# Optimization experiments

Measured on AMD Instinct MI355X. Metric: run time of the kernel, lower is better.

The kernel has to match this reference:

```python
import jax, jax.numpy as jnp
import numpy as np

H = 300          # node_hidden_dim (GINE output dim)
D = 2 * H        # set2set in_channels = 600
STEPS = 2        # num_step_set2_set


def _lstm_cell(x, h, c, W_ih, W_hh, b_ih, b_hh):
    # PyTorch LSTM gate order: i, f, g, o
    gates = x @ W_ih.T + h @ W_hh.T + b_ih + b_hh
    i, f, g, o = jnp.split(gates, 4, axis=-1)
    c = jax.nn.sigmoid(f) * c + jax.nn.sigmoid(i) * jnp.tanh(g)
    h = jax.nn.sigmoid(o) * jnp.tanh(c)
    return h, c


def _set2set(x, batch, num_graphs, W_ih, W_hh, b_ih, b_hh):
    # torch_geometric Set2Set with processing_steps=STEPS, 1-layer LSTM
    B = num_graphs
    q_star = jnp.zeros((B, 2 * D), x.dtype)
    h = jnp.zeros((B, D), x.dtype)
    c = jnp.zeros((B, D), x.dtype)
    for _ in range(STEPS):
        h, c = _lstm_cell(q_star, h, c, W_ih, W_hh, b_ih, b_hh)
        q = h                                   # [B, D]
        e = jnp.sum(x * q[batch], axis=-1)      # [N]
        emax = jax.ops.segment_max(e, batch, num_segments=B)
        a = jnp.exp(e - emax[batch])
        asum = jax.ops.segment_sum(a, batch, num_segments=B)
        a = a / (asum[batch] + 1e-16)           # segment softmax
        r = jax.ops.segment_sum(a[:, None] * x, batch, num_segments=B)
        q_star = jnp.concatenate([q, r], axis=-1)   # [B, 2D]
    return q_star


def _l2norm(x):
    return x / jnp.maximum(jnp.linalg.norm(x, axis=1, keepdims=True), 1e-12)


def setup_inputs() -> dict:
    key = jax.random.key(0)
    ks = jax.random.split(key, 8)
    Nu, Nv, B = 8192, 8192, 256
    solute_x = jax.random.normal(ks[0], (Nu, H), jnp.float32)
    solvent_x = jax.random.normal(ks[1], (Nv, H), jnp.float32)
    solute_batch = jnp.sort(jax.random.randint(ks[2], (Nu,), 0, B)).astype(jnp.int32)
    solvent_batch = jnp.sort(jax.random.randint(ks[3], (Nv,), 0, B)).astype(jnp.int32)
    lstm_W_ih = jax.random.normal(ks[4], (4 * D, 2 * D), jnp.float32) * 0.02
    lstm_W_hh = jax.random.normal(ks[5], (4 * D, D), jnp.float32) * 0.02
    lstm_b_ih = jnp.zeros((4 * D,), jnp.float32)
    lstm_b_hh = jnp.zeros((4 * D,), jnp.float32)
    pred_W = jax.random.normal(ks[6], (1, 8 * H), jnp.float32) * 0.02
    pred_b = jnp.zeros((1,), jnp.float32)
    return {
        "solute_x": solute_x, "solvent_x": solvent_x,
        "solute_batch": solute_batch, "solvent_batch": solvent_batch,
        "num_graphs": B,
        "lstm_W_ih": lstm_W_ih, "lstm_W_hh": lstm_W_hh,
        "lstm_b_ih": lstm_b_ih, "lstm_b_hh": lstm_b_hh,
        "pred_W": pred_W, "pred_b": pred_b,
    }


def reference(solute_x, solvent_x, solute_batch, solvent_batch, num_graphs,
              lstm_W_ih, lstm_W_hh, lstm_b_ih, lstm_b_hh, pred_W, pred_b):
    # F.normalize(dim=1)
    su = _l2norm(solute_x)    # [Nu, H]
    sv = _l2norm(solvent_x)   # [Nv, H]
    # len_map = solute_len.T @ solvent_len == same-pair membership mask
    mask = (solute_batch[:, None] == solvent_batch[None, :]).astype(su.dtype)
    interaction_map = (su @ sv.T) * mask          # [Nu, Nv]
    ret_interaction_map = interaction_map
    solvent_prime = interaction_map.T @ su        # [Nv, H]
    solute_prime = interaction_map @ sv           # [Nu, H]
    su2 = jnp.concatenate([su, solute_prime], axis=1)    # [Nu, 2H]
    sv2 = jnp.concatenate([sv, solvent_prime], axis=1)   # [Nv, 2H]
    su_s2s = _set2set(su2, solute_batch, num_graphs, lstm_W_ih, lstm_W_hh, lstm_b_ih, lstm_b_hh)
    sv_s2s = _set2set(sv2, solvent_batch, num_graphs, lstm_W_ih, lstm_W_hh, lstm_b_ih, lstm_b_hh)
    final = jnp.concatenate([su_s2s, sv_s2s], axis=1)    # [B, 8H]
    predictions = final @ pred_W.T + pred_b              # [B, 1]
    return predictions, ret_interaction_map
```

## Files before the change

kernel.cpp:

```cpp
#include <hip/hip_runtime.h>
#include <math.h>

#define HDIM 300
#define DDIM 600
#define NGR  256

typedef float vf4 __attribute__((ext_vector_type(4)));
typedef float vf2 __attribute__((ext_vector_type(2)));

__device__ __forceinline__ float wred_sum(float v){
  #pragma unroll
  for(int o=32;o;o>>=1) v += __shfl_xor(v,o,64);
  return v;
}
__device__ __forceinline__ float wred_max(float v){
  #pragma unroll
  for(int o=32;o;o>>=1) v = fmaxf(v,__shfl_xor(v,o,64));
  return v;
}
__device__ __forceinline__ float sigm(float x){ return 1.f/(1.f+expf(-x)); }

__device__ __forceinline__ void fill_row(int i, const int* __restrict__ ub,
    const int* __restrict__ voff, float* __restrict__ mapbase, int Nv, int tid){
  int g = ub[i];
  int js = voff[g], je = voff[g+1];
  float* mrow = mapbase + (size_t)i*Nv;
  const vf4 z4 = {0.f,0.f,0.f,0.f};
  int nf4 = Nv >> 2;
  for (int q4=tid; q4<nf4; q4+=256){
    int j0 = q4*4;
    if (j0+4 <= js || j0 >= je){
      __builtin_nontemporal_store(z4, (vf4*)(mrow + j0));
    } else {
      #pragma unroll
      for(int u=0;u<4;u++){ int j=j0+u; if (j<js || j>=je) mrow[j]=0.f; }
    }
  }
}

__global__ __launch_bounds__(256) void k_norm_off(const float* __restrict__ xu,
    const float* __restrict__ xv, float* __restrict__ su, float* __restrict__ sv,
    int Nu, int Nv, const int* __restrict__ ub, const int* __restrict__ vb,
    int* __restrict__ uoff, int* __restrict__ voff,
    const float* __restrict__ b_ih, const float* __restrict__ b_hh,
    float* __restrict__ h1, float* __restrict__ c1,
    const float* __restrict__ pb, float* __restrict__ outp,
    const float* __restrict__ Wih, const float* __restrict__ Whh,
    float* __restrict__ gbase){
  int NBn = (Nu + Nv) >> 2;
  int b = blockIdx.x;
  int tid = threadIdx.x, lane = tid & 63, w = tid >> 6;
  if (b == NBn){
    int t = tid;
    if (t < NGR){
      int lo=0, hi=Nu;
      while(lo<hi){ int m=(lo+hi)>>1; if (ub[m] < t) lo=m+1; else hi=m; }
      uoff[t]=lo;
      lo=0; hi=Nv;
      while(lo<hi){ int m=(lo+hi)>>1; if (vb[m] < t) lo=m+1; else hi=m; }
      voff[t]=lo;
      if (t==0){ uoff[NGR]=Nu; voff[NGR]=Nv; }
      outp[t] = pb[0];
    }
    for (int d=tid; d<DDIM; d+=256){
      float gi = b_ih[d]      + b_hh[d];
      float gg = b_ih[1200+d] + b_hh[1200+d];
      float go = b_ih[1800+d] + b_hh[1800+d];
      float c  = sigm(gi)*tanhf(gg);
      c1[d]=c; h1[d]=sigm(go)*tanhf(c);
    }
    return;
  }
  if (b > NBn){
    __shared__ float h1l[DDIM];
    for (int d=tid; d<DDIM; d+=256){
      float gi = b_ih[d]      + b_hh[d];
      float gg = b_ih[1200+d] + b_hh[1200+d];
      float go = b_ih[1800+d] + b_hh[1800+d];
      float c  = sigm(gi)*tanhf(gg);
      h1l[d]   = sigm(go)*tanhf(c);
    }
    __syncthreads();
    int n = (b - NBn - 1)*4 + w;
    const float* wi = Wih + (size_t)n*1200;
    const float* wh = Whh + (size_t)n*600;
    float s = 0.f;
    for (int k=lane; k<DDIM; k+=64) s += h1l[k]*(wi[k] + wh[k]);
    s = wred_sum(s);
    if (lane==0) gbase[n] = s + b_ih[n] + b_hh[n];
    return;
  }
  int wid = b*4 + w;
  const float* src; float* dst;
  if (wid < Nu){ src = xu + (size_t)wid*HDIM; dst = su + (size_t)wid*HDIM; }
  else         { src = xv + (size_t)(wid-Nu)*HDIM; dst = sv + (size_t)(wid-Nu)*HDIM; }
  const vf4* s4 = (const vf4*)src;
  vf4 A = s4[lane];
  vf4 Bv = (lane<11)? s4[64+lane] : (vf4){0.f,0.f,0.f,0.f};
  float s = A.x*A.x+A.y*A.y+A.z*A.z+A.w*A.w + Bv.x*Bv.x+Bv.y*Bv.y+Bv.z*Bv.z+Bv.w*Bv.w;
  s = wred_sum(s);
  float inv = 1.f / fmaxf(sqrtf(s), 1e-12f);
  vf4* d4 = (vf4*)dst;
  d4[lane] = A*inv;
  if (lane<11) d4[64+lane] = Bv*inv;
}

__global__ __launch_bounds__(256) void k_prime(const float* __restrict__ su,
    const float* __restrict__ sv, const int* __restrict__ ub,
    const int* __restrict__ vb, const int* __restrict__ uoff,
    const int* __restrict__ voff, float* __restrict__ spr,
    float* __restrict__ svp, float* __restrict__ e1u, float* __restrict__ e1v,
    const float* __restrict__ h1, float* __restrict__ mapbase, int Nu, int Nv){
  int b = blockIdx.x;
  int tid = threadIdx.x, lane = tid & 63, w = tid >> 6;
  int r = b % 3;
  if (r == 2){ fill_row(b/3, ub, voff, mapbase, Nv, tid); return; }
  int idx = (b/3)*2 + r;
  bool isU = (idx < Nu);
  int i = isU ? idx : idx - Nu;
  const float* xa = isU ? su : sv;
  const float* xb = isU ? sv : su;
  const int* mybatch = isU ? ub : vb;
  const int* ooff    = isU ? voff : uoff;
  float* prime = isU ? spr : svp;
  float* eout  = isU ? e1u : e1v;

  __shared__ __align__(16) float xrow[304];
  __shared__ __align__(16) float prl[4*304];
  __shared__ float qv[2*HDIM];
  __shared__ float red[4];
  const float* rowp = xa + (size_t)i*HDIM;
  for (int t=tid; t<HDIM;   t+=256) xrow[t] = rowp[t];
  for (int t=tid; t<2*HDIM; t+=256) qv[t]   = h1[t];
  int g = mybatch[i];
  int js = ooff[g], je = ooff[g+1];
  __syncthreads();

  const vf4* x4 = (const vf4*)xrow;
  vf4 xA = x4[lane];
  vf4 xB = (lane<11)? x4[64+lane] : (vf4){0.f,0.f,0.f,0.f};
  vf4 prA = {0.f,0.f,0.f,0.f}, prB = {0.f,0.f,0.f,0.f};
  for (int j = js + w; j < je; j += 4){
    const vf4* orow = (const vf4*)(xb + (size_t)j*HDIM);
    vf4 oA = orow[lane];
    vf4 oB = (lane<11)? orow[64+lane] : (vf4){0.f,0.f,0.f,0.f};
    float d = oA.x*xA.x + oA.y*xA.y + oA.z*xA.z + oA.w*xA.w
            + oB.x*xB.x + oB.y*xB.y + oB.z*xB.z + oB.w*xB.w;
    d = wred_sum(d);
    if (isU && lane==0) mapbase[(size_t)i*Nv + j] = d;
    prA += d * oA;
    prB += d * oB;
  }
  vf4* p4 = (vf4*)(prl + w*304);
  p4[lane] = prA;
  if (lane<11) p4[64+lane] = prB;
  __syncthreads();
  float ep = 0.f;
  for (int t=tid; t<HDIM; t+=256){
    float s = prl[t] + prl[304+t] + prl[608+t] + prl[912+t];
    prime[(size_t)i*HDIM + t] = s;
    ep += xrow[t]*qv[t] + s*qv[HDIM+t];
  }
  ep = wred_sum(ep);
  if (lane==0) red[w] = ep;
  __syncthreads();
  if (tid==0) eout[i] = red[0]+red[1]+red[2]+red[3];
}

__global__ __launch_bounds__(256) void k_r1(const float* __restrict__ su,
    const float* __restrict__ sv, const float* __restrict__ spr,
    const float* __restrict__ svp, const float* __restrict__ e1u,
    const float* __restrict__ e1v, const int* __restrict__ uoff,
    const int* __restrict__ voff, float* __restrict__ r1){
  int tid = threadIdx.x, lane = tid & 63, w = tid >> 6;
  int bs = blockIdx.x; int set = bs >> 8; int g = bs & 255;
  const float* x  = set? sv  : su;
  const float* pr = set? svp : spr;
  const float* e  = set? e1v : e1u;
  const int* off  = set? voff: uoff;
  __shared__ float al[2048]; __shared__ float red[4]; __shared__ float shv;
  int ns = off[g], ne = off[g+1]; int n = ne - ns;
  float m = -INFINITY;
  for (int t=ns+tid; t<ne; t+=256) m = fmaxf(m, e[t]);
  m = wred_max(m);
  if (lane==0) red[w]=m;
  __syncthreads();
  if (tid==0) shv = fmaxf(fmaxf(red[0],red[1]),fmaxf(red[2],red[3]));
  __syncthreads();
  float emax = shv;
  float s = 0.f;
  for (int t=tid; t<n; t+=256){ float a = expf(e[ns+t]-emax); if (t<2048) al[t]=a; s += a; }
  s = wred_sum(s);
  __syncthreads();
  if (lane==0) red[w]=s;
  __syncthreads();
  if (tid==0) shv = red[0]+red[1]+red[2]+red[3];
  __syncthreads();
  float inv = 1.f/(shv + 1e-16f);
  float acc[3] = {0.f,0.f,0.f};
  #pragma unroll 4
  for (int nn=0; nn<n; nn++){
    float a = (nn<2048)? al[nn] : expf(e[ns+nn]-emax);
    const float* xr = x  + (size_t)(ns+nn)*HDIM;
    const float* pp = pr + (size_t)(ns+nn)*HDIM;
    #pragma unroll
    for(int u=0;u<3;u++){ int c = tid + u*256; if (c<DDIM){
        float xv = (c<HDIM)? xr[c] : pp[c-HDIM]; acc[u] += a*xv; } }
  }
  #pragma unroll
  for(int u=0;u<3;u++){ int c = tid + u*256; if (c<DDIM) r1[(size_t)bs*DDIM + c] = acc[u]*inv; }
}

__global__ __launch_bounds__(256) void k_gemm_lstm(const float* __restrict__ r1,
    const float* __restrict__ Wih, const float* __restrict__ gbase,
    const float* __restrict__ c1, float* __restrict__ h2){
  __shared__ __align__(16) float smem[32*68];
  float* Al = smem;
  float* Bl = smem + 16*36;
  int tid = threadIdx.x;
  int d0  = blockIdx.x*16;
  int gs0 = blockIdx.y*32;
  int tx = tid & 15, ty = tid >> 4;
  float acc[2][4] = {};
  for (int kt=0; kt<600; kt+=16){
    int k = kt + tx;
    bool kok = (k < 600);
    #pragma unroll
    for (int u=0; u<2; u++){
      int rl = ty + u*16;
      Al[tx*36 + rl] = kok ? r1[(size_t)(gs0+rl)*DDIM + k] : 0.f;
    }
    #pragma unroll
    for (int u=0; u<4; u++){
      int cl = ty + u*16;
      int gate = cl >> 4, dd = cl & 15;
      int d = d0 + dd;
      Bl[tx*68 + cl] = (kok && d < 600)
          ? Wih[(size_t)(gate*600 + d)*1200 + 600 + k] : 0.f;
    }
    __syncthreads();
    #pragma unroll
    for (int kk=0; kk<16; kk++){
      vf2 av = ((const vf2*)(Al + kk*36))[ty];
      vf4 bv = ((const vf4*)(Bl + kk*68))[tx];
      float a[2]={av.x,av.y}, bb[4]={bv.x,bv.y,bv.z,bv.w};
      #pragma unroll
      for(int mm=0;mm<2;mm++)
        #pragma unroll
        for(int nn=0;nn<4;nn++) acc[mm][nn] += a[mm]*bb[nn];
    }
    __syncthreads();
  }
  #pragma unroll
  for (int mm=0; mm<2; mm++){
    vf4 o = {acc[mm][0], acc[mm][1], acc[mm][2], acc[mm][3]};
    ((vf4*)(smem + (ty*2+mm)*68))[tx] = o;
  }
  __syncthreads();
  int d_l = tid & 15, r0 = tid >> 4;
  int d = d0 + d_l;
  if (d < 600){
    float gb_i = gbase[d], gb_f = gbase[600+d], gb_g = gbase[1200+d], gb_o = gbase[1800+d];
    float cc1 = c1[d];
    #pragma unroll
    for (int u=0; u<2; u++){
      int rl = r0 + u*16;
      const float* gr = smem + rl*68;
      float gi = gr[d_l]      + gb_i;
      float gf = gr[16+d_l]   + gb_f;
      float gG = gr[32+d_l]   + gb_g;
      float go = gr[48+d_l]   + gb_o;
      float c  = sigm(gf)*cc1 + sigm(gi)*tanhf(gG);
      h2[(size_t)(gs0+rl)*DDIM + d] = sigm(go)*tanhf(c);
    }
  }
}

__global__ __launch_bounds__(256) void k_r2(const float* __restrict__ su,
    const float* __restrict__ sv, const float* __restrict__ spr,
    const float* __restrict__ svp, const int* __restrict__ uoff,
    const int* __restrict__ voff, const float* __restrict__ h2,
    const float* __restrict__ pW, float* __restrict__ e2u,
    float* __restrict__ e2v, float* __restrict__ outp){
  int tid = threadIdx.x, lane = tid & 63, w = tid >> 6;
  int bs = blockIdx.x; int set = bs >> 8; int g = bs & 255;
  const float* x  = set? sv  : su;
  const float* pr = set? svp : spr;
  const int* off  = set? voff: uoff;
  float* e2g      = set? e2v : e2u;
  __shared__ float q[DDIM]; __shared__ float e2l[128]; __shared__ float al[128];
  __shared__ float red[4]; __shared__ float shv;
  for (int t=tid; t<DDIM; t+=256) q[t] = h2[(size_t)bs*DDIM + t];
  int ns = off[g], ne = off[g+1]; int n = ne - ns;
  __syncthreads();
  #pragma unroll 2
  for (int node = ns + w; node < ne; node += 4){
    const float* xr = x  + (size_t)node*HDIM;
    const float* pp = pr + (size_t)node*HDIM;
    float d = 0.f;
    #pragma unroll
    for(int c=0;c<10;c++){ int k = lane + 64*c; if (k<DDIM){
        float xv = (k<HDIM)? xr[k] : pp[k-HDIM]; d += xv*q[k]; } }
    d = wred_sum(d);
    if (lane==0){ int t = node-ns; if (t<128) e2l[t] = d; else e2g[node] = d; }
  }
  __syncthreads();
  float m = -INFINITY;
  for (int t=tid; t<n; t+=256) m = fmaxf(m, (t<128)? e2l[t] : e2g[ns+t]);
  m = wred_max(m);
  if (lane==0) red[w]=m;
  __syncthreads();
  if (tid==0) shv = fmaxf(fmaxf(red[0],red[1]),fmaxf(red[2],red[3]));
  __syncthreads();
  float emax = shv;
  float s = 0.f;
  for (int t=tid; t<n; t+=256){
    float a = expf(((t<128)? e2l[t] : e2g[ns+t]) - emax);
    if (t<128) al[t]=a; else e2g[ns+t]=a;
    s += a;
  }
  s = wred_sum(s);
  __syncthreads();
  if (lane==0) red[w]=s;
  __syncthreads();
  if (tid==0) shv = red[0]+red[1]+red[2]+red[3];
  __syncthreads();
  float inv = 1.f/(shv + 1e-16f);
  float acc[3] = {0.f,0.f,0.f};
  #pragma unroll 4
  for (int nn=0; nn<n; nn++){
    float a = (nn<128)? al[nn] : e2g[ns+nn];
    const float* xr = x  + (size_t)(ns+nn)*HDIM;
    const float* pp = pr + (size_t)(ns+nn)*HDIM;
    #pragma unroll
    for(int u=0;u<3;u++){ int c = tid + u*256; if (c<DDIM){
        float xv = (c<HDIM)? xr[c] : pp[c-HDIM]; acc[u] += a*xv; } }
  }
  int hoff = set? 1200 : 0;
  float p = 0.f;
  #pragma unroll
  for(int u=0;u<3;u++){ int c = tid + u*256; if (c<DDIM) p += (acc[u]*inv)*pW[hoff+600+c]; }
  for (int t=tid; t<DDIM; t+=256) p += q[t]*pW[hoff+t];
  p = wred_sum(p);
  __syncthreads();
  if (lane==0) red[w] = p;
  __syncthreads();
  if (tid==0) atomicAdd(&outp[g], red[0]+red[1]+red[2]+red[3]);
}

extern "C" void kernel_launch(void* const* d_in, const int* in_sizes, int n_in,
                              void* d_out, int out_size, void* d_ws, size_t ws_size,
                              hipStream_t stream) {
  const float* solute_x  = (const float*)d_in[0];
  const float* solvent_x = (const float*)d_in[1];
  const int*   ub        = (const int*)d_in[2];
  const int*   vb        = (const int*)d_in[3];
  const float* Wih  = (const float*)d_in[5];
  const float* Whh  = (const float*)d_in[6];
  const float* b_ih = (const float*)d_in[7];
  const float* b_hh = (const float*)d_in[8];
  const float* pW   = (const float*)d_in[9];
  const float* pb   = (const float*)d_in[10];

  int Nu = in_sizes[0] / HDIM;
  int Nv = in_sizes[1] / HDIM;

  float* out = (float*)d_out;
  int predn = out_size - Nu*Nv;
  float* mapbase = out + predn;

  float* ws = (float*)d_ws;
  float* su    = ws;
  float* sv    = su    + (size_t)Nu*HDIM;
  float* spr   = sv    + (size_t)Nv*HDIM;
  float* svp   = spr   + (size_t)Nu*HDIM;
  float* e1u   = svp   + (size_t)Nv*HDIM;
  float* e1v   = e1u   + Nu;
  float* h1    = e1v   + Nv;
  float* c1    = h1    + DDIM;
  float* r1    = c1    + DDIM;
  float* gbase = r1    + 512*DDIM;
  float* h2    = gbase + 2400;
  int*   uoff  = (int*)(h2 + 512*DDIM);
  int*   voff  = uoff + 257;

  k_norm_off<<<dim3((Nu+Nv)/4 + 1 + 600), dim3(256), 0, stream>>>(
      solute_x, solvent_x, su, sv, Nu, Nv, ub, vb, uoff, voff,
      b_ih, b_hh, h1, c1, pb, out, Wih, Whh, gbase);
  k_prime<<<dim3(24576), dim3(256), 0, stream>>>(
      su, sv, ub, vb, uoff, voff, spr, svp, e1u, e1v, h1, mapbase, Nu, Nv);
  k_r1<<<dim3(512), dim3(256), 0, stream>>>(
      su, sv, spr, svp, e1u, e1v, uoff, voff, r1);
  k_gemm_lstm<<<dim3(38, 16), dim3(256), 0, stream>>>(r1, Wih, gbase, c1, h2);
  k_r2<<<dim3(512), dim3(256), 0, stream>>>(
      su, sv, spr, svp, uoff, voff, h2, pW, e1u, e1v, out);
}
```

Baseline: 520.9 us.

## Fuse per-row prime computation and first set2set readout into per-graph blocks

Replaces the per-row k_prime kernel and the per-graph k_r1 kernel with one k_graph kernel. Each of 512 compute blocks handles one graph of one set. It stages the partner graph's rows in shared memory in tiles of 32 and processes the block's own rows eight at a time, so partner rows are reused across many rows instead of being reloaded for each row. The same block then does the segment softmax and the first weighted readout, which removes a kernel launch and the global round trip of e1. Map-row filling blocks are interleaved into the same grid. The cost is only 512 large blocks plus long serial loops per graph, which can hurt occupancy and load balance, and the interleaving index arithmetic is intricate.

Measured after the change: 583.2 us. +12.0%, slower.

```diff
diff --git a/kernel.cpp b/kernel.cpp
--- a/kernel.cpp
+++ b/kernel.cpp
@@ -105,83 +105,152 @@
   if (lane<11) d4[64+lane] = Bv*inv;
 }
 
-__global__ __launch_bounds__(256) void k_prime(const float* __restrict__ su,
-    const float* __restrict__ sv, const int* __restrict__ ub,
-    const int* __restrict__ vb, const int* __restrict__ uoff,
-    const int* __restrict__ voff, float* __restrict__ spr,
-    float* __restrict__ svp, float* __restrict__ e1u, float* __restrict__ e1v,
-    const float* __restrict__ h1, float* __restrict__ mapbase, int Nu, int Nv){
+__global__ __launch_bounds__(256) void k_graph(
+    const float* __restrict__ su, const float* __restrict__ sv,
+    const int* __restrict__ ub,
+    const int* __restrict__ uoff, const int* __restrict__ voff,
+    float* __restrict__ spr, float* __restrict__ svp,
+    float* __restrict__ e1u, float* __restrict__ e1v,
+    const float* __restrict__ h1, float* __restrict__ mapbase,
+    float* __restrict__ r1, int Nv){
   int b = blockIdx.x;
   int tid = threadIdx.x, lane = tid & 63, w = tid >> 6;
-  int r = b % 3;
-  if (r == 2){ fill_row(b/3, ub, voff, mapbase, Nv, tid); return; }
-  int idx = (b/3)*2 + r;
-  bool isU = (idx < Nu);
-  int i = isU ? idx : idx - Nu;
-  const float* xa = isU ? su : sv;
-  const float* xb = isU ? sv : su;
-  const int* mybatch = isU ? ub : vb;
-  const int* ooff    = isU ? voff : uoff;
-  float* prime = isU ? spr : svp;
-  float* eout  = isU ? e1u : e1v;
-
-  __shared__ __align__(16) float xrow[304];
-  __shared__ __align__(16) float prl[4*304];
-  __shared__ float qv[2*HDIM];
+  int P = (gridDim.x + 511) >> 9;
+  int q = b / P;
+  if ((b % P) != 0 || q >= 512){
+    int nb_comp = (b % P) ? (q + 1) : q;
+    if (nb_comp > 512) nb_comp = 512;
+    fill_row(b - nb_comp, ub, voff, mapbase, Nv, tid);
+    return;
+  }
+  int cid = q;
+  int set = cid & 1, g = cid >> 1;
+  const float* xown = set ? sv  : su;
+  const float* xpar = set ? su  : sv;
+  const int*   ooff = set ? voff: uoff;
+  const int*   poff = set ? uoff: voff;
+  float* prime = set ? svp : spr;
+  float* e1g   = set ? e1v : e1u;
+  int us = ooff[g], ue = ooff[g+1];
+  int ps = poff[g], pe = poff[g+1];
+  int n = ue - us, np = pe - ps;
+
+  __shared__ __align__(16) float SVl[32*308];
+  __shared__ __align__(16) float XUl[8*308];
+  __shared__ __align__(16) float Ql[608];
+  __shared__ float e1l[256];
+  __shared__ float al[256];
   __shared__ float red[4];
-  const float* rowp = xa + (size_t)i*HDIM;
-  for (int t=tid; t<HDIM;   t+=256) xrow[t] = rowp[t];
-  for (int t=tid; t<2*HDIM; t+=256) qv[t]   = h1[t];
-  int g = mybatch[i];
-  int js = ooff[g], je = ooff[g+1];
-  __syncthreads();
-
-  const vf4* x4 = (const vf4*)xrow;
-  vf4 xA = x4[lane];
-  vf4 xB = (lane<11)? x4[64+lane] : (vf4){0.f,0.f,0.f,0.f};
-  vf4 prA = {0.f,0.f,0.f,0.f}, prB = {0.f,0.f,0.f,0.f};
-  for (int j = js + w; j < je; j += 4){
-    const vf4* orow = (const vf4*)(xb + (size_t)j*HDIM);
-    vf4 oA = orow[lane];
-    vf4 oB = (lane<11)? orow[64+lane] : (vf4){0.f,0.f,0.f,0.f};
-    float d = oA.x*xA.x + oA.y*xA.y + oA.z*xA.z + oA.w*xA.w
-            + oB.x*xB.x + oB.y*xB.y + oB.z*xB.z + oB.w*xB.w;
-    d = wred_sum(d);
-    if (isU && lane==0) mapbase[(size_t)i*Nv + j] = d;
-    prA += d * oA;
-    prB += d * oB;
-  }
-  vf4* p4 = (vf4*)(prl + w*304);
-  p4[lane] = prA;
-  if (lane<11) p4[64+lane] = prB;
-  __syncthreads();
-  float ep = 0.f;
-  for (int t=tid; t<HDIM; t+=256){
-    float s = prl[t] + prl[304+t] + prl[608+t] + prl[912+t];
-    prime[(size_t)i*HDIM + t] = s;
-    ep += xrow[t]*qv[t] + s*qv[HDIM+t];
-  }
-  ep = wred_sum(ep);
-  if (lane==0) red[w] = ep;
-  __syncthreads();
-  if (tid==0) eout[i] = red[0]+red[1]+red[2]+red[3];
-}
-
-__global__ __launch_bounds__(256) void k_r1(const float* __restrict__ su,
-    const float* __restrict__ sv, const float* __restrict__ spr,
-    const float* __restrict__ svp, const float* __restrict__ e1u,
-    const float* __restrict__ e1v, const int* __restrict__ uoff,
-    const int* __restrict__ voff, float* __restrict__ r1){
-  int tid = threadIdx.x, lane = tid & 63, w = tid >> 6;
-  int bs = blockIdx.x; int set = bs >> 8; int g = bs & 255;
-  const float* x  = set? sv  : su;
-  const float* pr = set? svp : spr;
-  const float* e  = set? e1v : e1u;
-  const int* off  = set? voff: uoff;
-  __shared__ float al[2048]; __shared__ float red[4]; __shared__ float shv;
-  int ns = off[g], ne = off[g+1]; int n = ne - ns;
+  __shared__ float shv;
+
+  for (int t=tid; t<DDIM; t+=256) Ql[t] = h1[t];
+  bool single = (np <= 32);
+  if (single){
+    for (int idx=tid; idx<np*HDIM; idx+=256){
+      int r = idx/HDIM, c = idx - r*HDIM;
+      SVl[r*308+c] = xpar[(size_t)(ps+r)*HDIM + c];
+    }
+  }
+  const vf4* SV4 = (const vf4*)SVl;
+  const vf4* XU4 = (const vf4*)XUl;
+  const vf4* Q4  = (const vf4*)Ql;
+  int jj = lane & 31, half = lane >> 5;
+
+  int passes = (n + 7) >> 3;
+  for (int p=0; p<passes; p++){
+    int i0 = us + p*8;
+    int nr = min(8, ue - i0);
+    __syncthreads();
+    for (int idx=tid; idx<nr*HDIM; idx+=256){
+      int r = idx/HDIM, c = idx - r*HDIM;
+      XUl[r*308+c] = xown[(size_t)(i0+r)*HDIM + c];
+    }
+    if (!single){
+      int nc0 = np < 32 ? np : 32;
+      for (int idx=tid; idx<nc0*HDIM; idx+=256){
+        int r = idx/HDIM, c = idx - r*HDIM;
+        SVl[r*308+c] = xpar[(size_t)(ps+r)*HDIM + c];
+      }
+    }
+    __syncthreads();
+
+    int lr = 2*w + half;
+    int gi = i0 + lr;
+    bool rv = (lr < nr);
+    vf4 prA0={0,0,0,0}, prB0={0,0,0,0}, prA1={0,0,0,0}, prB1={0,0,0,0};
+
+    for (int cs = ps, ci = 0; cs < pe; cs += 32, ci++){
+      int nc = min(32, pe - cs);
+      if (!single && ci > 0){
+        __syncthreads();
+        for (int idx=tid; idx<nc*HDIM; idx+=256){
+          int r = idx/HDIM, c = idx - r*HDIM;
+          SVl[r*308+c] = xpar[(size_t)(cs+r)*HDIM + c];
+        }
+        __syncthreads();
+      }
+      float d = 0.f;
+      const vf4* svr = SV4 + jj*77;
+      const vf4* xr4 = XU4 + lr*77;
+      for (int c4=0; c4<75; c4++){
+        vf4 s4 = svr[c4], x4 = xr4[c4];
+        d += s4.x*x4.x + s4.y*x4.y + s4.z*x4.z + s4.w*x4.w;
+      }
+      if (set==0 && rv && jj<nc) mapbase[(size_t)gi*Nv + (cs+jj)] = d;
+      for (int j=0; j<nc; j++){
+        float d0 = __shfl(d, j);
+        float d1 = __shfl(d, 32+j);
+        vf4 sA = SV4[j*77 + lane];
+        vf4 sB = (lane<11)? SV4[j*77 + 64 + lane] : (vf4){0,0,0,0};
+        prA0 += d0*sA; prB0 += d0*sB;
+        prA1 += d1*sA; prB1 += d1*sB;
+      }
+    }
+
+    int r0 = 2*w;
+    bool rv0 = (r0   < nr);
+    bool rv1 = (r0+1 < nr);
+    if (rv0){
+      int gi0 = i0 + r0;
+      vf4 xA = XU4[r0*77 + lane];
+      vf4 qA = Q4[lane], q2A = Q4[75+lane];
+      float ep = xA.x*qA.x+xA.y*qA.y+xA.z*qA.z+xA.w*qA.w
+               + prA0.x*q2A.x+prA0.y*q2A.y+prA0.z*q2A.z+prA0.w*q2A.w;
+      if (lane<11){
+        vf4 xB = XU4[r0*77+64+lane];
+        vf4 qB = Q4[64+lane], q2B = Q4[139+lane];
+        ep += xB.x*qB.x+xB.y*qB.y+xB.z*qB.z+xB.w*qB.w
+            + prB0.x*q2B.x+prB0.y*q2B.y+prB0.z*q2B.z+prB0.w*q2B.w;
+      }
+      ep = wred_sum(ep);
+      vf4* p4 = (vf4*)(prime + (size_t)gi0*HDIM);
+      p4[lane] = prA0;
+      if (lane<11) p4[64+lane] = prB0;
+      if (lane==0){ int t = gi0-us; if (t<256) e1l[t]=ep; else e1g[gi0]=ep; }
+    }
+    if (rv1){
+      int gi1 = i0 + r0 + 1;
+      vf4 xA = XU4[(r0+1)*77 + lane];
+      vf4 qA = Q4[lane], q2A = Q4[75+lane];
+      float ep = xA.x*qA.x+xA.y*qA.y+xA.z*qA.z+xA.w*qA.w
+               + prA1.x*q2A.x+prA1.y*q2A.y+prA1.z*q2A.z+prA1.w*q2A.w;
+      if (lane<11){
+        vf4 xB = XU4[(r0+1)*77+64+lane];
+        vf4 qB = Q4[64+lane], q2B = Q4[139+lane];
+        ep += xB.x*qB.x+xB.y*qB.y+xB.z*qB.z+xB.w*qB.w
+            + prB1.x*q2B.x+prB1.y*q2B.y+prB1.z*q2B.z+prB1.w*q2B.w;
+      }
+      ep = wred_sum(ep);
+      vf4* p4 = (vf4*)(prime + (size_t)gi1*HDIM);
+      p4[lane] = prA1;
+      if (lane<11) p4[64+lane] = prB1;
+      if (lane==0){ int t = gi1-us; if (t<256) e1l[t]=ep; else e1g[gi1]=ep; }
+    }
+  }
+
+  __syncthreads();
   float m = -INFINITY;
-  for (int t=ns+tid; t<ne; t+=256) m = fmaxf(m, e[t]);
+  for (int t=tid; t<n; t+=256) m = fmaxf(m, (t<256)? e1l[t] : e1g[us+t]);
   m = wred_max(m);
   if (lane==0) red[w]=m;
   __syncthreads();
@@ -189,7 +258,11 @@
   __syncthreads();
   float emax = shv;
   float s = 0.f;
-  for (int t=tid; t<n; t+=256){ float a = expf(e[ns+t]-emax); if (t<2048) al[t]=a; s += a; }
+  for (int t=tid; t<n; t+=256){
+    float a = expf(((t<256)? e1l[t] : e1g[us+t]) - emax);
+    if (t<256) al[t]=a; else e1g[us+t]=a;
+    s += a;
+  }
   s = wred_sum(s);
   __syncthreads();
   if (lane==0) red[w]=s;
@@ -200,13 +273,14 @@
   float acc[3] = {0.f,0.f,0.f};
   #pragma unroll 4
   for (int nn=0; nn<n; nn++){
-    float a = (nn<2048)? al[nn] : expf(e[ns+nn]-emax);
-    const float* xr = x  + (size_t)(ns+nn)*HDIM;
-    const float* pp = pr + (size_t)(ns+nn)*HDIM;
+    float a = (nn<256)? al[nn] : e1g[us+nn];
+    const float* xr = xown  + (size_t)(us+nn)*HDIM;
+    const float* pp = prime + (size_t)(us+nn)*HDIM;
     #pragma unroll
     for(int u=0;u<3;u++){ int c = tid + u*256; if (c<DDIM){
         float xv = (c<HDIM)? xr[c] : pp[c-HDIM]; acc[u] += a*xv; } }
   }
+  int bs = (set<<8) | g;
   #pragma unroll
   for(int u=0;u<3;u++){ int c = tid + u*256; if (c<DDIM) r1[(size_t)bs*DDIM + c] = acc[u]*inv; }
 }
@@ -387,10 +461,8 @@
   k_norm_off<<<dim3((Nu+Nv)/4 + 1 + 600), dim3(256), 0, stream>>>(
       solute_x, solvent_x, su, sv, Nu, Nv, ub, vb, uoff, voff,
       b_ih, b_hh, h1, c1, pb, out, Wih, Whh, gbase);
-  k_prime<<<dim3(24576), dim3(256), 0, stream>>>(
-      su, sv, ub, vb, uoff, voff, spr, svp, e1u, e1v, h1, mapbase, Nu, Nv);
-  k_r1<<<dim3(512), dim3(256), 0, stream>>>(
-      su, sv, spr, svp, e1u, e1v, uoff, voff, r1);
+  k_graph<<<dim3(Nu + 512), dim3(256), 0, stream>>>(
+      su, sv, ub, uoff, voff, spr, svp, e1u, e1v, h1, mapbase, r1, Nv);
   k_gemm_lstm<<<dim3(38, 16), dim3(256), 0, stream>>>(r1, Wih, gbase, c1, h2);
   k_r2<<<dim3(512), dim3(256), 0, stream>>>(
       su, sv, spr, svp, uoff, voff, h2, pW, e1u, e1v, out);
```

## Process two rows per wave with lane-parallel dot products in pair kernel

Applied to the files above, without the earlier changes.

Replaces the per-row prime kernel with a pair kernel in which each wave handles two consecutive rows. The dot products are computed one partner row per lane, then broadcast with shuffles to accumulate the prime vectors, so each partner row load is shared by both rows. Blocks that fill map rows are interleaved with compute blocks. The goal is to cut repeated partner loads and the per-dot wave reductions, at the cost of strided per-lane loads and more divergence when a row pair straddles two graphs.

After: 569.1 us. 9.3% more time.

```diff
diff --git a/kernel.cpp b/kernel.cpp
--- a/kernel.cpp
+++ b/kernel.cpp
@@ -105,66 +105,106 @@
   if (lane<11) d4[64+lane] = Bv*inv;
 }
 
-__global__ __launch_bounds__(256) void k_prime(const float* __restrict__ su,
-    const float* __restrict__ sv, const int* __restrict__ ub,
-    const int* __restrict__ vb, const int* __restrict__ uoff,
-    const int* __restrict__ voff, float* __restrict__ spr,
-    float* __restrict__ svp, float* __restrict__ e1u, float* __restrict__ e1v,
-    const float* __restrict__ h1, float* __restrict__ mapbase, int Nu, int Nv){
-  int b = blockIdx.x;
-  int tid = threadIdx.x, lane = tid & 63, w = tid >> 6;
-  int r = b % 3;
-  if (r == 2){ fill_row(b/3, ub, voff, mapbase, Nv, tid); return; }
-  int idx = (b/3)*2 + r;
-  bool isU = (idx < Nu);
-  int i = isU ? idx : idx - Nu;
-  const float* xa = isU ? su : sv;
-  const float* xb = isU ? sv : su;
-  const int* mybatch = isU ? ub : vb;
-  const int* ooff    = isU ? voff : uoff;
-  float* prime = isU ? spr : svp;
-  float* eout  = isU ? e1u : e1v;
-
-  __shared__ __align__(16) float xrow[304];
-  __shared__ __align__(16) float prl[4*304];
-  __shared__ float qv[2*HDIM];
-  __shared__ float red[4];
-  const float* rowp = xa + (size_t)i*HDIM;
-  for (int t=tid; t<HDIM;   t+=256) xrow[t] = rowp[t];
-  for (int t=tid; t<2*HDIM; t+=256) qv[t]   = h1[t];
-  int g = mybatch[i];
-  int js = ooff[g], je = ooff[g+1];
-  __syncthreads();
-
-  const vf4* x4 = (const vf4*)xrow;
-  vf4 xA = x4[lane];
-  vf4 xB = (lane<11)? x4[64+lane] : (vf4){0.f,0.f,0.f,0.f};
-  vf4 prA = {0.f,0.f,0.f,0.f}, prB = {0.f,0.f,0.f,0.f};
-  for (int j = js + w; j < je; j += 4){
-    const vf4* orow = (const vf4*)(xb + (size_t)j*HDIM);
-    vf4 oA = orow[lane];
-    vf4 oB = (lane<11)? orow[64+lane] : (vf4){0.f,0.f,0.f,0.f};
-    float d = oA.x*xA.x + oA.y*xA.y + oA.z*xA.z + oA.w*xA.w
-            + oB.x*xB.x + oB.y*xB.y + oB.z*xB.z + oB.w*xB.w;
-    d = wred_sum(d);
-    if (isU && lane==0) mapbase[(size_t)i*Nv + j] = d;
-    prA += d * oA;
-    prB += d * oB;
-  }
-  vf4* p4 = (vf4*)(prl + w*304);
-  p4[lane] = prA;
-  if (lane<11) p4[64+lane] = prB;
-  __syncthreads();
-  float ep = 0.f;
-  for (int t=tid; t<HDIM; t+=256){
-    float s = prl[t] + prl[304+t] + prl[608+t] + prl[912+t];
-    prime[(size_t)i*HDIM + t] = s;
-    ep += xrow[t]*qv[t] + s*qv[HDIM+t];
-  }
-  ep = wred_sum(ep);
-  if (lane==0) red[w] = ep;
-  __syncthreads();
-  if (tid==0) eout[i] = red[0]+red[1]+red[2]+red[3];
+__global__ __launch_bounds__(256) void k_pair(
+    const float* __restrict__ su, const float* __restrict__ sv,
+    const int* __restrict__ ub, const int* __restrict__ vb,
+    const int* __restrict__ uoff, const int* __restrict__ voff,
+    float* __restrict__ spr, float* __restrict__ svp,
+    float* __restrict__ e1u, float* __restrict__ e1v,
+    const float* __restrict__ h1, float* __restrict__ mapbase,
+    int Nu, int Nv){
+  int b = blockIdx.x, tid = threadIdx.x, lane = tid & 63, w = tid >> 6;
+  int ncomp = (Nu + Nv) >> 3;
+  int P = gridDim.x / ncomp;
+  int q = b / P;
+  if ((b % P) != 0 || q >= ncomp){
+    int nb = (b % P) ? (q + 1) : q;
+    if (nb > ncomp) nb = ncomp;
+    fill_row(b - nb, ub, voff, mapbase, Nv, tid);
+    return;
+  }
+  int p  = q*4 + w;
+  int r0 = 2*p;
+  bool isU = (r0 < Nu);
+  int i0 = isU ? r0 : r0 - Nu;
+  const float* xown = isU ? su : sv;
+  const float* xpar = isU ? sv : su;
+  const int* batch  = isU ? ub : vb;
+  const int* poff   = isU ? voff : uoff;
+  float* prime      = isU ? spr : svp;
+  float* e1g        = isU ? e1u : e1v;
+
+  __shared__ __align__(16) float XS[4][2*308];
+  float* X = XS[w];
+  for (int t=lane; t<2*HDIM; t+=64){
+    int rr = t / HDIM, c = t - rr*HDIM;
+    X[rr*308 + c] = xown[(size_t)i0*HDIM + t];
+  }
+  int g0 = batch[i0], g1 = batch[i0+1];
+  int ngrp = (g0==g1) ? 1 : 2;
+  const vf4* H4  = (const vf4*)h1;
+  const vf4* H4b = (const vf4*)(h1 + HDIM);
+
+  for (int grp=0; grp<ngrp; grp++){
+    int g  = grp ? g1 : g0;
+    int rA = (ngrp==2) ? grp : 0;
+    int has2 = (ngrp==1) ? 1 : 0;
+    int ps = poff[g], pe = poff[g+1];
+    const vf4* X0 = (const vf4*)(X + rA*308);
+    const vf4* X1 = (const vf4*)(X + (rA+1)*308);
+    vf4 pA0={0,0,0,0}, pB0={0,0,0,0}, pA1={0,0,0,0}, pB1={0,0,0,0};
+    for (int cs=ps; cs<pe; cs+=64){
+      int nc = min(64, pe-cs);
+      float d0 = 0.f, d1 = 0.f;
+      if (lane < nc){
+        const vf4* pr = (const vf4*)(xpar + (size_t)(cs+lane)*HDIM);
+        #pragma unroll 5
+        for (int c4=0; c4<75; c4++){
+          vf4 pv = pr[c4];
+          vf4 x0 = X0[c4];
+          d0 += pv.x*x0.x + pv.y*x0.y + pv.z*x0.z + pv.w*x0.w;
+          if (has2){
+            vf4 x1 = X1[c4];
+            d1 += pv.x*x1.x + pv.y*x1.y + pv.z*x1.z + pv.w*x1.w;
+          }
+        }
+      }
+      if (isU && lane < nc){
+        mapbase[(size_t)(i0+rA)*Nv + (cs+lane)] = d0;
+        if (has2) mapbase[(size_t)(i0+rA+1)*Nv + (cs+lane)] = d1;
+      }
+      for (int j=0; j<nc; j++){
+        float dj0 = __shfl(d0, j);
+        float dj1 = has2 ? __shfl(d1, j) : 0.f;
+        const vf4* pr = (const vf4*)(xpar + (size_t)(cs+j)*HDIM);
+        vf4 a  = pr[lane];
+        vf4 bb = (lane<11) ? pr[64+lane] : (vf4){0.f,0.f,0.f,0.f};
+        pA0 += dj0*a; pB0 += dj0*bb;
+        if (has2){ pA1 += dj1*a; pB1 += dj1*bb; }
+      }
+    }
+    for (int rr=0; rr<=has2; rr++){
+      int irow = i0 + rA + rr;
+      vf4 pA = rr ? pA1 : pA0;
+      vf4 pB = rr ? pB1 : pB0;
+      vf4* pp = (vf4*)(prime + (size_t)irow*HDIM);
+      pp[lane] = pA;
+      if (lane<11) pp[64+lane] = pB;
+      const vf4* Xr = (const vf4*)(X + (rA+rr)*308);
+      vf4 xo = Xr[lane];
+      vf4 q1 = H4[lane], q2 = H4b[lane];
+      float ep = xo.x*q1.x+xo.y*q1.y+xo.z*q1.z+xo.w*q1.w
+               + pA.x*q2.x+pA.y*q2.y+pA.z*q2.z+pA.w*q2.w;
+      if (lane<11){
+        vf4 xo2 = Xr[64+lane];
+        vf4 q1b = H4[64+lane], q2b = H4b[64+lane];
+        ep += xo2.x*q1b.x+xo2.y*q1b.y+xo2.z*q1b.z+xo2.w*q1b.w
+            + pB.x*q2b.x+pB.y*q2b.y+pB.z*q2b.z+pB.w*q2b.w;
+      }
+      ep = wred_sum(ep);
+      if (lane==0) e1g[irow] = ep;
+    }
+  }
 }
 
 __global__ __launch_bounds__(256) void k_r1(const float* __restrict__ su,
@@ -387,7 +427,7 @@
   k_norm_off<<<dim3((Nu+Nv)/4 + 1 + 600), dim3(256), 0, stream>>>(
       solute_x, solvent_x, su, sv, Nu, Nv, ub, vb, uoff, voff,
       b_ih, b_hh, h1, c1, pb, out, Wih, Whh, gbase);
-  k_prime<<<dim3(24576), dim3(256), 0, stream>>>(
+  k_pair<<<dim3((Nu+Nv)/8 + Nu), dim3(256), 0, stream>>>(
       su, sv, ub, vb, uoff, voff, spr, svp, e1u, e1v, h1, mapbase, Nu, Nv);
   k_r1<<<dim3(512), dim3(256), 0, stream>>>(
       su, sv, spr, svp, e1u, e1v, uoff, voff, r1);
```

## Fuse five kernel stages into one cooperative persistent kernel with grid syncs

Applied to the files above, without the earlier changes.

Replaces the five separate launches (normalize/offsets, prime/interaction map, r1, LSTM GEMM, r2) with one cooperative kernel of 1024 blocks. The blocks loop over virtual block indices and separate the stages with grid-wide syncs. The aim is to remove launch overhead and the gaps between kernels. In exchange, occupancy is capped by the cooperative grid size and the large stages run as grid-stride loops, which may balance load worse. The original multi-launch path is kept as a fallback if the cooperative launch fails.

After: 1.048 ms. 101% more time.

```diff
diff --git a/kernel.cpp b/kernel.cpp
--- a/kernel.cpp
+++ b/kernel.cpp
@@ -1,9 +1,12 @@
 #include <hip/hip_runtime.h>
+#include <hip/hip_cooperative_groups.h>
 #include <math.h>
 
 #define HDIM 300
 #define DDIM 600
 #define NGR  256
+
+namespace cg = cooperative_groups;
 
 typedef float vf4 __attribute__((ext_vector_type(4)));
 typedef float vf2 __attribute__((ext_vector_type(2)));
@@ -35,6 +38,315 @@
       #pragma unroll
       for(int u=0;u<4;u++){ int j=j0+u; if (j<js || j>=je) mrow[j]=0.f; }
     }
+  }
+}
+
+struct KP {
+  const float* xu; const float* xv;
+  const int* bu; const int* bv;
+  const float* Wih; const float* Whh; const float* b_ih; const float* b_hh;
+  const float* pW; const float* pb;
+  float* su; float* sv; float* spr; float* svp;
+  float* e1u; float* e1v; float* h1; float* c1;
+  float* r1; float* gbase; float* h2;
+  int* uoff; int* voff;
+  float* outp; float* mapbase;
+  int Nu; int Nv;
+};
+
+__global__ __launch_bounds__(256,4) void k_all(KP P){
+  cg::grid_group gg = cg::this_grid();
+  __shared__ __align__(16) float smem[2180];
+  int tid = threadIdx.x, lane = tid & 63, w = tid >> 6;
+  int NBn = (P.Nu + P.Nv) >> 2;
+  int nA = NBn + 1 + 600;
+
+  for (int vb = blockIdx.x; vb < nA; vb += gridDim.x){
+    if (vb == NBn){
+      int t = tid;
+      if (t < NGR){
+        int lo=0, hi=P.Nu;
+        while(lo<hi){ int m=(lo+hi)>>1; if (P.bu[m] < t) lo=m+1; else hi=m; }
+        P.uoff[t]=lo;
+        lo=0; hi=P.Nv;
+        while(lo<hi){ int m=(lo+hi)>>1; if (P.bv[m] < t) lo=m+1; else hi=m; }
+        P.voff[t]=lo;
+        if (t==0){ P.uoff[NGR]=P.Nu; P.voff[NGR]=P.Nv; }
+        P.outp[t] = P.pb[0];
+      }
+      for (int d=tid; d<DDIM; d+=256){
+        float gi = P.b_ih[d]      + P.b_hh[d];
+        float gg2= P.b_ih[1200+d] + P.b_hh[1200+d];
+        float go = P.b_ih[1800+d] + P.b_hh[1800+d];
+        float c  = sigm(gi)*tanhf(gg2);
+        P.c1[d]=c; P.h1[d]=sigm(go)*tanhf(c);
+      }
+    } else if (vb > NBn){
+      float* h1l = smem;
+      for (int d=tid; d<DDIM; d+=256){
+        float gi = P.b_ih[d]      + P.b_hh[d];
+        float gg2= P.b_ih[1200+d] + P.b_hh[1200+d];
+        float go = P.b_ih[1800+d] + P.b_hh[1800+d];
+        float c  = sigm(gi)*tanhf(gg2);
+        h1l[d]   = sigm(go)*tanhf(c);
+      }
+      __syncthreads();
+      int n = (vb - NBn - 1)*4 + w;
+      const float* wi = P.Wih + (size_t)n*1200;
+      const float* wh = P.Whh + (size_t)n*600;
+      float s = 0.f;
+      for (int k=lane; k<DDIM; k+=64) s += h1l[k]*(wi[k] + wh[k]);
+      s = wred_sum(s);
+      if (lane==0) P.gbase[n] = s + P.b_ih[n] + P.b_hh[n];
+      __syncthreads();
+    } else {
+      int wid = vb*4 + w;
+      const float* src; float* dst;
+      if (wid < P.Nu){ src = P.xu + (size_t)wid*HDIM; dst = P.su + (size_t)wid*HDIM; }
+      else           { src = P.xv + (size_t)(wid-P.Nu)*HDIM; dst = P.sv + (size_t)(wid-P.Nu)*HDIM; }
+      const vf4* s4 = (const vf4*)src;
+      vf4 A = s4[lane];
+      vf4 Bv = (lane<11)? s4[64+lane] : (vf4){0.f,0.f,0.f,0.f};
+      float s = A.x*A.x+A.y*A.y+A.z*A.z+A.w*A.w + Bv.x*Bv.x+Bv.y*Bv.y+Bv.z*Bv.z+Bv.w*Bv.w;
+      s = wred_sum(s);
+      float inv = 1.f / fmaxf(sqrtf(s), 1e-12f);
+      vf4* d4 = (vf4*)dst;
+      d4[lane] = A*inv;
+      if (lane<11) d4[64+lane] = Bv*inv;
+    }
+  }
+  gg.sync();
+
+  int nB = P.Nu + P.Nv + P.Nu;
+  for (int vb = blockIdx.x; vb < nB; vb += gridDim.x){
+    int r = vb % 3;
+    if (r == 2){ fill_row(vb/3, P.bu, P.voff, P.mapbase, P.Nv, tid); continue; }
+    int idx = (vb/3)*2 + r;
+    bool isU = (idx < P.Nu);
+    int i = isU ? idx : idx - P.Nu;
+    const float* xa = isU ? P.su : P.sv;
+    const float* xb = isU ? P.sv : P.su;
+    const int* mybatch = isU ? P.bu : P.bv;
+    const int* ooff    = isU ? P.voff : P.uoff;
+    float* prime = isU ? P.spr : P.svp;
+    float* eout  = isU ? P.e1u : P.e1v;
+
+    float* xrow = smem;
+    float* prl  = smem + 304;
+    float* qv   = smem + 1520;
+    float* red  = smem + 2120;
+    const float* rowp = xa + (size_t)i*HDIM;
+    for (int t=tid; t<HDIM;   t+=256) xrow[t] = rowp[t];
+    for (int t=tid; t<2*HDIM; t+=256) qv[t]   = P.h1[t];
+    int g = mybatch[i];
+    int js = ooff[g], je = ooff[g+1];
+    __syncthreads();
+
+    const vf4* x4 = (const vf4*)xrow;
+    vf4 xA = x4[lane];
+    vf4 xB = (lane<11)? x4[64+lane] : (vf4){0.f,0.f,0.f,0.f};
+    vf4 prA = {0.f,0.f,0.f,0.f}, prB = {0.f,0.f,0.f,0.f};
+    for (int j = js + w; j < je; j += 4){
+      const vf4* orow = (const vf4*)(xb + (size_t)j*HDIM);
+      vf4 oA = orow[lane];
+      vf4 oB = (lane<11)? orow[64+lane] : (vf4){0.f,0.f,0.f,0.f};
+      float d = oA.x*xA.x + oA.y*xA.y + oA.z*xA.z + oA.w*xA.w
+              + oB.x*xB.x + oB.y*xB.y + oB.z*xB.z + oB.w*xB.w;
+      d = wred_sum(d);
+      if (isU && lane==0) P.mapbase[(size_t)i*P.Nv + j] = d;
+      prA += d * oA;
+      prB += d * oB;
+    }
+    vf4* p4 = (vf4*)(prl + w*304);
+    p4[lane] = prA;
+    if (lane<11) p4[64+lane] = prB;
+    __syncthreads();
+    float ep = 0.f;
+    for (int t=tid; t<HDIM; t+=256){
+      float s = prl[t] + prl[304+t] + prl[608+t] + prl[912+t];
+      prime[(size_t)i*HDIM + t] = s;
+      ep += xrow[t]*qv[t] + s*qv[HDIM+t];
+    }
+    ep = wred_sum(ep);
+    if (lane==0) red[w] = ep;
+    __syncthreads();
+    if (tid==0) eout[i] = red[0]+red[1]+red[2]+red[3];
+  }
+  gg.sync();
+
+  for (int vb = blockIdx.x; vb < 2*NGR; vb += gridDim.x){
+    int set = vb >> 8; int g = vb & 255;
+    const float* x  = set? P.sv  : P.su;
+    const float* pr = set? P.svp : P.spr;
+    const float* e  = set? P.e1v : P.e1u;
+    const int* off  = set? P.voff: P.uoff;
+    float* al  = smem;
+    float* red = smem + 2048;
+    float* shv = smem + 2052;
+    int ns = off[g], ne = off[g+1]; int n = ne - ns;
+    float m = -INFINITY;
+    for (int t=ns+tid; t<ne; t+=256) m = fmaxf(m, e[t]);
+    m = wred_max(m);
+    if (lane==0) red[w]=m;
+    __syncthreads();
+    if (tid==0) *shv = fmaxf(fmaxf(red[0],red[1]),fmaxf(red[2],red[3]));
+    __syncthreads();
+    float emax = *shv;
+    float s = 0.f;
+    for (int t=tid; t<n; t+=256){ float a = expf(e[ns+t]-emax); if (t<2048) al[t]=a; s += a; }
+    s = wred_sum(s);
+    __syncthreads();
+    if (lane==0) red[w]=s;
+    __syncthreads();
+    if (tid==0) *shv = red[0]+red[1]+red[2]+red[3];
+    __syncthreads();
+    float inv = 1.f/(*shv + 1e-16f);
+    float acc[3] = {0.f,0.f,0.f};
+    #pragma unroll 4
+    for (int nn=0; nn<n; nn++){
+      float a = (nn<2048)? al[nn] : expf(e[ns+nn]-emax);
+      const float* xr = x  + (size_t)(ns+nn)*HDIM;
+      const float* pp = pr + (size_t)(ns+nn)*HDIM;
+      #pragma unroll
+      for(int u=0;u<3;u++){ int c = tid + u*256; if (c<DDIM){
+          float xv = (c<HDIM)? xr[c] : pp[c-HDIM]; acc[u] += a*xv; } }
+    }
+    #pragma unroll
+    for(int u=0;u<3;u++){ int c = tid + u*256; if (c<DDIM) P.r1[(size_t)vb*DDIM + c] = acc[u]*inv; }
+    __syncthreads();
+  }
+  gg.sync();
+
+  for (int vb = blockIdx.x; vb < 38*16; vb += gridDim.x){
+    float* Al = smem;
+    float* Bl = smem + 16*36;
+    int d0  = (vb % 38)*16;
+    int gs0 = (vb / 38)*32;
+    int tx = tid & 15, ty = tid >> 4;
+    float acc[2][4] = {};
+    for (int kt=0; kt<600; kt+=16){
+      int k = kt + tx;
+      bool kok = (k < 600);
+      #pragma unroll
+      for (int u=0; u<2; u++){
+        int rl = ty + u*16;
+        Al[tx*36 + rl] = kok ? P.r1[(size_t)(gs0+rl)*DDIM + k] : 0.f;
+      }
+      #pragma unroll
+      for (int u=0; u<4; u++){
+        int cl = ty + u*16;
+        int gate = cl >> 4, dd = cl & 15;
+        int d = d0 + dd;
+        Bl[tx*68 + cl] = (kok && d < 600)
+            ? P.Wih[(size_t)(gate*600 + d)*1200 + 600 + k] : 0.f;
+      }
+      __syncthreads();
+      #pragma unroll
+      for (int kk=0; kk<16; kk++){
+        vf2 av = ((const vf2*)(Al + kk*36))[ty];
+        vf4 bv = ((const vf4*)(Bl + kk*68))[tx];
+        float a[2]={av.x,av.y}, bb[4]={bv.x,bv.y,bv.z,bv.w};
+        #pragma unroll
+        for(int mm=0;mm<2;mm++)
+          #pragma unroll
+          for(int nn=0;nn<4;nn++) acc[mm][nn] += a[mm]*bb[nn];
+      }
+      __syncthreads();
+    }
+    #pragma unroll
+    for (int mm=0; mm<2; mm++){
+      vf4 o = {acc[mm][0], acc[mm][1], acc[mm][2], acc[mm][3]};
+      ((vf4*)(smem + (ty*2+mm)*68))[tx] = o;
+    }
+    __syncthreads();
+    int d_l = tid & 15, rr0 = tid >> 4;
+    int d = d0 + d_l;
+    if (d < 600){
+      float gb_i = P.gbase[d], gb_f = P.gbase[600+d], gb_g = P.gbase[1200+d], gb_o = P.gbase[1800+d];
+      float cc1 = P.c1[d];
+      #pragma unroll
+      for (int u=0; u<2; u++){
+        int rl = rr0 + u*16;
+        const float* gr = smem + rl*68;
+        float gi = gr[d_l]      + gb_i;
+        float gf = gr[16+d_l]   + gb_f;
+        float gG = gr[32+d_l]   + gb_g;
+        float go = gr[48+d_l]   + gb_o;
+        float c  = sigm(gf)*cc1 + sigm(gi)*tanhf(gG);
+        P.h2[(size_t)(gs0+rl)*DDIM + d] = sigm(go)*tanhf(c);
+      }
+    }
+    __syncthreads();
+  }
+  gg.sync();
+
+  for (int vb = blockIdx.x; vb < 2*NGR; vb += gridDim.x){
+    int set = vb >> 8; int g = vb & 255;
+    const float* x  = set? P.sv  : P.su;
+    const float* pr = set? P.svp : P.spr;
+    const int* off  = set? P.voff: P.uoff;
+    float* e2g      = set? P.e1v : P.e1u;
+    float* ql  = smem;
+    float* e2l = smem + 600;
+    float* al  = smem + 728;
+    float* red = smem + 856;
+    float* shv = smem + 860;
+    for (int t=tid; t<DDIM; t+=256) ql[t] = P.h2[(size_t)vb*DDIM + t];
+    int ns = off[g], ne = off[g+1]; int n = ne - ns;
+    __syncthreads();
+    #pragma unroll 2
+    for (int node = ns + w; node < ne; node += 4){
+      const float* xr = x  + (size_t)node*HDIM;
+      const float* pp = pr + (size_t)node*HDIM;
+      float d = 0.f;
+      #pragma unroll
+      for(int c=0;c<10;c++){ int k = lane + 64*c; if (k<DDIM){
+          float xv = (k<HDIM)? xr[k] : pp[k-HDIM]; d += xv*ql[k]; } }
+      d = wred_sum(d);
+      if (lane==0){ int t = node-ns; if (t<128) e2l[t] = d; else e2g[node] = d; }
+    }
+    __syncthreads();
+    float m = -INFINITY;
+    for (int t=tid; t<n; t+=256) m = fmaxf(m, (t<128)? e2l[t] : e2g[ns+t]);
+    m = wred_max(m);
+    if (lane==0) red[w]=m;
+    __syncthreads();
+    if (tid==0) *shv = fmaxf(fmaxf(red[0],red[1]),fmaxf(red[2],red[3]));
+    __syncthreads();
+    float emax = *shv;
+    float s = 0.f;
+    for (int t=tid; t<n; t+=256){
+      float a = expf(((t<128)? e2l[t] : e2g[ns+t]) - emax);
+      if (t<128) al[t]=a; else e2g[ns+t]=a;
+      s += a;
+    }
+    s = wred_sum(s);
+    __syncthreads();
+    if (lane==0) red[w]=s;
+    __syncthreads();
+    if (tid==0) *shv = red[0]+red[1]+red[2]+red[3];
+    __syncthreads();
+    float inv = 1.f/(*shv + 1e-16f);
+    float acc[3] = {0.f,0.f,0.f};
+    #pragma unroll 4
+    for (int nn=0; nn<n; nn++){
+      float a = (nn<128)? al[nn] : e2g[ns+nn];
+      const float* xr = x  + (size_t)(ns+nn)*HDIM;
+      const float* pp = pr + (size_t)(ns+nn)*HDIM;
+      #pragma unroll
+      for(int u=0;u<3;u++){ int c = tid + u*256; if (c<DDIM){
+          float xv = (c<HDIM)? xr[c] : pp[c-HDIM]; acc[u] += a*xv; } }
+    }
+    int hoff = set? 1200 : 0;
+    float p = 0.f;
+    #pragma unroll
+    for(int u=0;u<3;u++){ int c = tid + u*256; if (c<DDIM) p += (acc[u]*inv)*P.pW[hoff+600+c]; }
+    for (int t=tid; t<DDIM; t+=256) p += ql[t]*P.pW[hoff+t];
+    p = wred_sum(p);
+    __syncthreads();
+    if (lane==0) red[w] = p;
+    __syncthreads();
+    if (tid==0) atomicAdd(&P.outp[g], red[0]+red[1]+red[2]+red[3]);
   }
 }
 
@@ -384,14 +696,30 @@
   int*   uoff  = (int*)(h2 + 512*DDIM);
   int*   voff  = uoff + 257;
 
-  k_norm_off<<<dim3((Nu+Nv)/4 + 1 + 600), dim3(256), 0, stream>>>(
-      solute_x, solvent_x, su, sv, Nu, Nv, ub, vb, uoff, voff,
-      b_ih, b_hh, h1, c1, pb, out, Wih, Whh, gbase);
-  k_prime<<<dim3(24576), dim3(256), 0, stream>>>(
-      su, sv, ub, vb, uoff, voff, spr, svp, e1u, e1v, h1, mapbase, Nu, Nv);
-  k_r1<<<dim3(512), dim3(256), 0, stream>>>(
-      su, sv, spr, svp, e1u, e1v, uoff, voff, r1);
-  k_gemm_lstm<<<dim3(38, 16), dim3(256), 0, stream>>>(r1, Wih, gbase, c1, h2);
-  k_r2<<<dim3(512), dim3(256), 0, stream>>>(
-      su, sv, spr, svp, uoff, voff, h2, pW, e1u, e1v, out);
-}
+  KP kp;
+  kp.xu = solute_x; kp.xv = solvent_x; kp.bu = ub; kp.bv = vb;
+  kp.Wih = Wih; kp.Whh = Whh; kp.b_ih = b_ih; kp.b_hh = b_hh;
+  kp.pW = pW; kp.pb = pb;
+  kp.su = su; kp.sv = sv; kp.spr = spr; kp.svp = svp;
+  kp.e1u = e1u; kp.e1v = e1v; kp.h1 = h1; kp.c1 = c1;
+  kp.r1 = r1; kp.gbase = gbase; kp.h2 = h2;
+  kp.uoff = uoff; kp.voff = voff;
+  kp.outp = out; kp.mapbase = mapbase;
+  kp.Nu = Nu; kp.Nv = Nv;
+
+  void* args[] = { (void*)&kp };
+  hipError_t err = hipLaunchCooperativeKernel((const void*)k_all,
+      dim3(1024), dim3(256), args, 0, stream);
+  if (err != hipSuccess){
+    k_norm_off<<<dim3((Nu+Nv)/4 + 1 + 600), dim3(256), 0, stream>>>(
+        solute_x, solvent_x, su, sv, Nu, Nv, ub, vb, uoff, voff,
+        b_ih, b_hh, h1, c1, pb, out, Wih, Whh, gbase);
+    k_prime<<<dim3(Nu + Nv + Nu), dim3(256), 0, stream>>>(
+        su, sv, ub, vb, uoff, voff, spr, svp, e1u, e1v, h1, mapbase, Nu, Nv);
+    k_r1<<<dim3(512), dim3(256), 0, stream>>>(
+        su, sv, spr, svp, e1u, e1v, uoff, voff, r1);
+    k_gemm_lstm<<<dim3(38, 16), dim3(256), 0, stream>>>(r1, Wih, gbase, c1, h2);
+    k_r2<<<dim3(512), dim3(256), 0, stream>>>(
+        su, sv, spr, svp, uoff, voff, h2, pW, e1u, e1v, out);
+  }
+}
```
